# Kernel optimization log

Measured on AMD Instinct MI355X. Metric: run time of the kernel, lower is better.

The kernel has to match this reference:

```python
import jax, jax.numpy as jnp
import numpy as np

B, S, D, H = 4, 2048, 1024, 16
HD = D // H  # head_dim = 64


def setup_inputs() -> dict:
    key = jax.random.key(0)
    ks = jax.random.split(key, 9)
    sc = 1.0 / np.sqrt(D)
    return {
        "x": jax.random.normal(ks[0], (B, S, D), dtype=jnp.float32),
        "Wq": jax.random.normal(ks[1], (D, D), dtype=jnp.float32) * sc,
        "bq": jnp.zeros((D,), dtype=jnp.float32),
        "Wk": jax.random.normal(ks[2], (D, D), dtype=jnp.float32) * sc,
        "bk": jnp.zeros((D,), dtype=jnp.float32),
        "Wv": jax.random.normal(ks[3], (D, D), dtype=jnp.float32) * sc,
        "bv": jnp.zeros((D,), dtype=jnp.float32),
        "Wo": jax.random.normal(ks[4], (D, D), dtype=jnp.float32) * sc,
        "bo": jnp.zeros((D,), dtype=jnp.float32),
    }


def reference(x, Wq, bq, Wk, bk, Wv, bv, Wo, bo):
    # QKV projections (torch Linear: x @ W.T + b), reshape to [B, H, S, HD]
    def proj(W, b):
        return (x @ W.T + b).reshape(B, S, H, HD).transpose(0, 2, 1, 3)

    Q, K, V = proj(Wq, bq), proj(Wk, bk), proj(Wv, bv)
    scores = jnp.einsum("bhqd,bhkd->bhqk", Q, K) / jnp.sqrt(jnp.float32(HD))
    attn = jax.nn.softmax(scores, axis=-1)  # dropout is identity at eval
    ctx = jnp.einsum("bhqk,bhkd->bhqd", attn, V)
    ctx = ctx.transpose(0, 2, 1, 3).reshape(B, S, D)
    out = ctx @ Wo.T + bo
    return out, attn
```

## Files before the change

### kernel.cpp

```cpp
#include <hip/hip_runtime.h>
#include <stdint.h>

#define Mm 8192
#define Dd 1024

typedef unsigned short u16;
typedef __attribute__((ext_vector_type(8))) short bf16x8;
typedef __attribute__((ext_vector_type(4))) float f32x4;
typedef __attribute__((ext_vector_type(4))) u16 u16x4;

__device__ __forceinline__ u16 f2bf(float f) {
  union { float f; uint32_t u; } c; c.f = f;
  uint32_t u = c.u;
  return (u16)((u + 0x7fffu + ((u >> 16) & 1u)) >> 16);
}

__device__ __forceinline__ float EXP2(float x) {
#if __has_builtin(__builtin_amdgcn_exp2f)
  return __builtin_amdgcn_exp2f(x);
#else
  return exp2f(x);
#endif
}

__device__ __forceinline__ float LOG2(float x) {
#if __has_builtin(__builtin_amdgcn_logf)
  return __builtin_amdgcn_logf(x);
#else
  return log2f(x);
#endif
}

__device__ __forceinline__ uint32_t cvtpk(float a, float b) {
  uint32_t r;
  asm("v_cvt_pk_bf16_f32 %0, %1, %2" : "=v"(r) : "v"(a), "v"(b));
  return r;
}

__device__ __forceinline__ void gll16(const void* g, void* l) {
  __builtin_amdgcn_global_load_lds((const __attribute__((address_space(1))) void*)g,
                                   (__attribute__((address_space(3))) void*)l, 16, 0, 0);
}

__global__ void cvt_all(const float* __restrict__ x, const float* __restrict__ wq,
                        const float* __restrict__ wk, const float* __restrict__ wv,
                        const float* __restrict__ wo, u16* __restrict__ out) {
  const int xn4 = 2097152, wn4 = 262144;
  const int total = xn4 + 4 * wn4;
  int i = blockIdx.x * blockDim.x + threadIdx.x;
  int stride = gridDim.x * blockDim.x;
  for (; i < total; i += stride) {
    const float* src; int off;
    if (i < xn4) { src = x; off = i; }
    else {
      int j = i - xn4; int wsel = j >> 18; off = j & (wn4 - 1);
      src = (wsel == 0) ? wq : (wsel == 1) ? wk : (wsel == 2) ? wv : wo;
    }
    float4 v = ((const float4*)src)[off];
    u16x4 o;
    o.x = f2bf(v.x); o.y = f2bf(v.y); o.z = f2bf(v.z); o.w = f2bf(v.w);
    ((u16x4*)out)[i] = o;
  }
}

__global__ __launch_bounds__(256) void gemm_qkv(
    const u16* __restrict__ A, const u16* __restrict__ Wt,
    const float* __restrict__ bq, const float* __restrict__ bk, const float* __restrict__ bv,
    u16* __restrict__ Qo, u16* __restrict__ Ko, u16* __restrict__ Vo, float qscale)
{
  __shared__ u16 As[128 * 32];
  __shared__ u16 Bs[128 * 32];
  const int K = 1024, tiles_n = 24;
  int nwg = 64 * 24;
  int bid = blockIdx.x;
  { int q = nwg >> 3; bid = (bid & 7) * q + (bid >> 3); }
  int tm = bid / tiles_n, tn = bid % tiles_n;
  int tid = threadIdx.x;
  int wid = tid >> 6, lane = tid & 63;
  int wr = wid >> 1, wc = wid & 1;

  f32x4 acc[4][4] = {};
  int a_row = wr * 64 + (lane & 15);
  int b_row = wc * 64 + (lane & 15);
  int frag_k = (lane >> 4) * 8;

  const u16* ga0 = A + (size_t)(tm * 128 + wid * 32 + (lane >> 2)) * K + (lane & 3) * 8;
  const u16* ga1 = ga0 + (size_t)16 * K;
  const u16* gb0 = Wt + (size_t)(tn * 128 + wid * 32 + (lane >> 2)) * K + (lane & 3) * 8;
  const u16* gb1 = gb0 + (size_t)16 * K;
  u16* lA0 = As + wid * 1024;
  u16* lA1 = As + wid * 1024 + 512;
  u16* lB0 = Bs + wid * 1024;
  u16* lB1 = Bs + wid * 1024 + 512;

  for (int kt = 0; kt < K; kt += 32) {
    gll16(ga0 + kt, lA0);
    gll16(ga1 + kt, lA1);
    gll16(gb0 + kt, lB0);
    gll16(gb1 + kt, lB1);
    __syncthreads();
    bf16x8 af[4], bfr[4];
#pragma unroll
    for (int i = 0; i < 4; i++)
      af[i] = *(const bf16x8*)(As + (a_row + i * 16) * 32 + frag_k);
#pragma unroll
    for (int i = 0; i < 4; i++)
      bfr[i] = *(const bf16x8*)(Bs + (b_row + i * 16) * 32 + frag_k);
#pragma unroll
    for (int i = 0; i < 4; i++)
#pragma unroll
      for (int j = 0; j < 4; j++)
        acc[i][j] = __builtin_amdgcn_mfma_f32_16x16x32_bf16(af[i], bfr[j], acc[i][j], 0, 0, 0);
    __syncthreads();
  }

#pragma unroll
  for (int i = 0; i < 4; i++) {
#pragma unroll
    for (int j = 0; j < 4; j++) {
      int col = tn * 128 + wc * 64 + j * 16 + (lane & 15);
      int wsel = col >> 10, c10 = col & 1023;
      int h = c10 >> 6, hd = c10 & 63;
      float bvv = (wsel == 0 ? bq : wsel == 1 ? bk : bv)[c10];
      int row0 = tm * 128 + wr * 64 + i * 16 + (lane >> 4) * 4;
      int b_ = row0 >> 11, s0 = row0 & 2047;
      if (wsel == 2) {
        u16x4 o;
#pragma unroll
        for (int r = 0; r < 4; r++) o[r] = f2bf(acc[i][j][r] + bvv);
        *(u16x4*)&Vo[((size_t)(b_ * 16 + h) * 64 + hd) * 2048 + s0] = o;
      } else {
        u16* dst = (wsel == 0) ? Qo : Ko;
        float sc = (wsel == 0) ? qscale : 1.0f;
#pragma unroll
        for (int r = 0; r < 4; r++)
          dst[(((size_t)(b_ * 16 + h) * 2048 + (s0 + r)) << 6) + hd] = f2bf((acc[i][j][r] + bvv) * sc);
      }
    }
  }
}

__global__ __launch_bounds__(256) void gemm_out(
    const u16* __restrict__ A, const u16* __restrict__ Bt,
    const float* __restrict__ bias, float* __restrict__ out,
    int M, int N, int K)
{
  __shared__ u16 As[128 * 32];
  __shared__ u16 Bs[128 * 32];
  int tiles_n = N >> 7;
  int nwg = (M >> 7) * tiles_n;
  int bid = blockIdx.x;
  { int q = nwg >> 3; bid = (bid & 7) * q + (bid >> 3); }
  int tm = bid / tiles_n, tn = bid % tiles_n;
  int tid = threadIdx.x;
  int wid = tid >> 6, lane = tid & 63;
  int wr = wid >> 1, wc = wid & 1;

  f32x4 acc[4][4] = {};
  int a_row = wr * 64 + (lane & 15);
  int b_row = wc * 64 + (lane & 15);
  int frag_k = (lane >> 4) * 8;

  const u16* ga0 = A + (size_t)(tm * 128 + wid * 32 + (lane >> 2)) * K + (lane & 3) * 8;
  const u16* ga1 = ga0 + (size_t)16 * K;
  const u16* gb0 = Bt + (size_t)(tn * 128 + wid * 32 + (lane >> 2)) * K + (lane & 3) * 8;
  const u16* gb1 = gb0 + (size_t)16 * K;
  u16* lA0 = As + wid * 1024;
  u16* lA1 = As + wid * 1024 + 512;
  u16* lB0 = Bs + wid * 1024;
  u16* lB1 = Bs + wid * 1024 + 512;

  for (int kt = 0; kt < K; kt += 32) {
    gll16(ga0 + kt, lA0);
    gll16(ga1 + kt, lA1);
    gll16(gb0 + kt, lB0);
    gll16(gb1 + kt, lB1);
    __syncthreads();
    bf16x8 af[4], bfr[4];
#pragma unroll
    for (int i = 0; i < 4; i++)
      af[i] = *(const bf16x8*)(As + (a_row + i * 16) * 32 + frag_k);
#pragma unroll
    for (int i = 0; i < 4; i++)
      bfr[i] = *(const bf16x8*)(Bs + (b_row + i * 16) * 32 + frag_k);
#pragma unroll
    for (int i = 0; i < 4; i++)
#pragma unroll
      for (int j = 0; j < 4; j++)
        acc[i][j] = __builtin_amdgcn_mfma_f32_16x16x32_bf16(af[i], bfr[j], acc[i][j], 0, 0, 0);
    __syncthreads();
  }

#pragma unroll
  for (int i = 0; i < 4; i++)
#pragma unroll
    for (int j = 0; j < 4; j++) {
      int col = tn * 128 + wc * 64 + j * 16 + (lane & 15);
      float bv = bias[col];
#pragma unroll
      for (int r = 0; r < 4; r++) {
        int row = tm * 128 + wr * 64 + i * 16 + (lane >> 4) * 4 + r;
        out[(size_t)row * N + col] = acc[i][j][r] + bv;
      }
    }
}

__global__ __launch_bounds__(512, 4) void attn_fused16q2(
    const u16* __restrict__ Qb, const u16* __restrict__ Kb,
    const u16* __restrict__ Vtb, float* __restrict__ attn_out,
    u16* __restrict__ ctxb)
{
  __shared__ u16 Ks[4][4096];
  __shared__ u16 Vs[4][4096];
  __shared__ u16 Ps[8192];

  int bid = blockIdx.x;
  int swz = (bid & 7) * 64 + (bid >> 3);
  int bh = swz >> 3, qtb = swz & 7;
  int tid = threadIdx.x, w = tid >> 6, lane = tid & 63;
  int g = lane >> 4, l15 = lane & 15;

  const u16* Kg = Kb + (size_t)bh * 2048 * 64;
  const u16* Vg = Vtb + (size_t)bh * 64 * 2048;
  const u16* Qg = Qb + ((size_t)bh * 2048 + qtb * 256) * 64;
  float* Ag = attn_out + ((size_t)bh * 2048 + qtb * 256) * 2048;

  int qloc = w * 16 + l15;
  bf16x8 aqA0 = *(const bf16x8*)(Qg + (size_t)qloc * 64 + g * 8);
  bf16x8 aqA1 = *(const bf16x8*)(Qg + (size_t)qloc * 64 + 32 + g * 8);
  bf16x8 aqB0 = *(const bf16x8*)(Qg + (size_t)(128 + qloc) * 64 + g * 8);
  bf16x8 aqB1 = *(const bf16x8*)(Qg + (size_t)(128 + qloc) * 64 + 32 + g * 8);

  int srow = w * 8 + (lane >> 3);
  int schunk = (lane & 7) ^ (lane >> 3);
  const u16* Ksrc = Kg + (size_t)srow * 64 + schunk * 8;
  const u16* Vsrc = Vg + (size_t)srow * 2048 + schunk * 8;

  int xq = (qloc & 7) << 4;
  char* Pb = (char*)Ps + qloc * 128;

  float eA0 = 0.f, eA1 = 0.f, eB0 = 0.f, eB1 = 0.f;
#pragma unroll
  for (int p = 0; p < 3; p++)
    gll16(Ksrc + (size_t)p * 4096, (char*)Ks[p] + w * 1024);
  for (int it = 0; it < 32; ++it) {
    if (it < 29) gll16(Ksrc + (size_t)(it + 3) * 4096, (char*)Ks[(it + 3) & 3] + w * 1024);
    if (it < 29)       asm volatile("s_waitcnt vmcnt(3)" ::: "memory");
    else if (it == 29) asm volatile("s_waitcnt vmcnt(2)" ::: "memory");
    else if (it == 30) asm volatile("s_waitcnt vmcnt(1)" ::: "memory");
    else               asm volatile("s_waitcnt vmcnt(0)" ::: "memory");
    __builtin_amdgcn_s_barrier();
    const char* Kbase = (const char*)Ks[it & 3];
    f32x4 sA[4] = {}, sB[4] = {};
    __builtin_amdgcn_s_setprio(1);
#pragma unroll
    for (int t = 0; t < 4; t++) {
      int kr = t * 16 + l15;
      int x = (kr & 7) << 4;
      bf16x8 k0 = *(const bf16x8*)(Kbase + kr * 128 + ((g * 16) ^ x));
      bf16x8 k1 = *(const bf16x8*)(Kbase + kr * 128 + ((64 + g * 16) ^ x));
      sA[t] = __builtin_amdgcn_mfma_f32_16x16x32_bf16(k0, aqA0, sA[t], 0, 0, 0);
      sA[t] = __builtin_amdgcn_mfma_f32_16x16x32_bf16(k1, aqA1, sA[t], 0, 0, 0);
      sB[t] = __builtin_amdgcn_mfma_f32_16x16x32_bf16(k0, aqB0, sB[t], 0, 0, 0);
      sB[t] = __builtin_amdgcn_mfma_f32_16x16x32_bf16(k1, aqB1, sB[t], 0, 0, 0);
    }
    __builtin_amdgcn_s_setprio(0);
#pragma unroll
    for (int t = 0; t < 4; t++)
#pragma unroll
      for (int r = 0; r < 4; r++) {
        if (t & 1) { eA1 += EXP2(sA[t][r]); eB1 += EXP2(sB[t][r]); }
        else       { eA0 += EXP2(sA[t][r]); eB0 += EXP2(sB[t][r]); }
      }
    asm volatile("" ::: "memory");
    __builtin_amdgcn_s_barrier();
  }
  float lsA = eA0 + eA1, lsB = eB0 + eB1;
  lsA += __shfl_xor(lsA, 16); lsA += __shfl_xor(lsA, 32);
  lsB += __shfl_xor(lsB, 16); lsB += __shfl_xor(lsB, 32);
  float lrA = -LOG2(lsA), lrB = -LOG2(lsB);

  f32x4 cA[4] = {}, cB[4] = {};
#pragma unroll
  for (int p = 0; p < 3; p++) {
    gll16(Ksrc + (size_t)p * 4096, (char*)Ks[p] + w * 1024);
    gll16(Vsrc + (size_t)p * 64,  (char*)Vs[p] + w * 1024);
  }
  for (int it = 0; it < 32; ++it) {
    if (it < 29) {
      gll16(Ksrc + (size_t)(it + 3) * 4096, (char*)Ks[(it + 3) & 3] + w * 1024);
      gll16(Vsrc + (size_t)(it + 3) * 64,  (char*)Vs[(it + 3) & 3] + w * 1024);
    }
    if (it == 0)      asm volatile("s_waitcnt vmcnt(6)" ::: "memory");
    else if (it == 1) asm volatile("s_waitcnt vmcnt(14)" ::: "memory");
    else if (it == 2) asm volatile("s_waitcnt vmcnt(22)" ::: "memory");
    else if (it < 29) asm volatile("s_waitcnt vmcnt(30)" ::: "memory");
    else if (it == 29) asm volatile("s_waitcnt vmcnt(28)" ::: "memory");
    else if (it == 30) asm volatile("s_waitcnt vmcnt(26)" ::: "memory");
    else               asm volatile("s_waitcnt vmcnt(24)" ::: "memory");
    __builtin_amdgcn_s_barrier();
    const char* Kbase = (const char*)Ks[it & 3];
    const char* Vbase = (const char*)Vs[it & 3];
    f32x4 sA[4] = {}, sB[4] = {};
    __builtin_amdgcn_s_setprio(1);
#pragma unroll
    for (int t = 0; t < 4; t++) {
      int kr = t * 16 + l15;
      int x = (kr & 7) << 4;
      bf16x8 k0 = *(const bf16x8*)(Kbase + kr * 128 + ((g * 16) ^ x));
      bf16x8 k1 = *(const bf16x8*)(Kbase + kr * 128 + ((64 + g * 16) ^ x));
      sA[t] = __builtin_amdgcn_mfma_f32_16x16x32_bf16(k0, aqA0, sA[t], 0, 0, 0);
      sA[t] = __builtin_amdgcn_mfma_f32_16x16x32_bf16(k1, aqA1, sA[t], 0, 0, 0);
      sB[t] = __builtin_amdgcn_mfma_f32_16x16x32_bf16(k0, aqB0, sB[t], 0, 0, 0);
      sB[t] = __builtin_amdgcn_mfma_f32_16x16x32_bf16(k1, aqB1, sB[t], 0, 0, 0);
    }
    __builtin_amdgcn_s_setprio(0);

    {
      float* Arow = Ag + (size_t)qloc * 2048 + it * 64 + g * 4;
#pragma unroll
      for (int t = 0; t < 4; t++) {
        f32x4 p;
#pragma unroll
        for (int r = 0; r < 4; r++) p[r] = EXP2(sA[t][r] + lrA);
        __builtin_nontemporal_store(p, (f32x4*)(Arow + t * 16));
        uint2 pk;
        pk.x = cvtpk(p[0], p[1]);
        pk.y = cvtpk(p[2], p[3]);
        *(uint2*)(Pb + ((t * 32 + g * 8) ^ xq)) = pk;
      }
      __builtin_amdgcn_s_setprio(1);
#pragma unroll
      for (int kk = 0; kk < 2; kk++) {
        bf16x8 ap = *(const bf16x8*)(Pb + ((kk * 64 + g * 16) ^ xq));
#pragma unroll
        for (int t = 0; t < 4; t++) {
          int dr = t * 16 + l15;
          bf16x8 bv = *(const bf16x8*)(Vbase + dr * 128 + ((kk * 64 + g * 16) ^ ((dr & 7) << 4)));
          cA[t] = __builtin_amdgcn_mfma_f32_16x16x32_bf16(ap, bv, cA[t], 0, 0, 0);
        }
      }
      __builtin_amdgcn_s_setprio(0);
    }
    {
      float* Arow = Ag + (size_t)(128 + qloc) * 2048 + it * 64 + g * 4;
#pragma unroll
      for (int t = 0; t < 4; t++) {
        f32x4 p;
#pragma unroll
        for (int r = 0; r < 4; r++) p[r] = EXP2(sB[t][r] + lrB);
        __builtin_nontemporal_store(p, (f32x4*)(Arow + t * 16));
        uint2 pk;
        pk.x = cvtpk(p[0], p[1]);
        pk.y = cvtpk(p[2], p[3]);
        *(uint2*)(Pb + ((t * 32 + g * 8) ^ xq)) = pk;
      }
      __builtin_amdgcn_s_setprio(1);
#pragma unroll
      for (int kk = 0; kk < 2; kk++) {
        bf16x8 ap = *(const bf16x8*)(Pb + ((kk * 64 + g * 16) ^ xq));
#pragma unroll
        for (int t = 0; t < 4; t++) {
          int dr = t * 16 + l15;
          bf16x8 bv = *(const bf16x8*)(Vbase + dr * 128 + ((kk * 64 + g * 16) ^ ((dr & 7) << 4)));
          cB[t] = __builtin_amdgcn_mfma_f32_16x16x32_bf16(ap, bv, cB[t], 0, 0, 0);
        }
      }
      __builtin_amdgcn_s_setprio(0);
    }
    asm volatile("" ::: "memory");
    __builtin_amdgcn_s_barrier();
  }

  int b_ = bh >> 4, h = bh & 15;
#pragma unroll
  for (int t = 0; t < 4; t++)
#pragma unroll
    for (int r = 0; r < 4; r++) {
      int qgA = qtb * 256 + w * 16 + g * 4 + r;
      int col = h * 64 + t * 16 + l15;
      ctxb[((size_t)b_ * 2048 + qgA) * 1024 + col] = f2bf(cA[t][r]);
      ctxb[((size_t)b_ * 2048 + qgA + 128) * 1024 + col] = f2bf(cB[t][r]);
    }
}

extern "C" void kernel_launch(void* const* d_in, const int* in_sizes, int n_in,
                              void* d_out, int out_size, void* d_ws, size_t ws_size,
                              hipStream_t stream) {
  const float* x  = (const float*)d_in[0];
  const float* Wq = (const float*)d_in[1];
  const float* bq = (const float*)d_in[2];
  const float* Wk = (const float*)d_in[3];
  const float* bk = (const float*)d_in[4];
  const float* Wv = (const float*)d_in[5];
  const float* bv = (const float*)d_in[6];
  const float* Wo = (const float*)d_in[7];
  const float* bo = (const float*)d_in[8];

  u16* xb   = (u16*)d_ws;
  u16* Wqb  = xb + (size_t)Mm * Dd;
  u16* Wkb  = Wqb + (size_t)Dd * Dd;
  u16* Wvb  = Wkb + (size_t)Dd * Dd;
  u16* Wob  = Wvb + (size_t)Dd * Dd;
  u16* Qb   = Wob + (size_t)Dd * Dd;
  u16* Kbuf = Qb + (size_t)Mm * Dd;
  u16* Vtb  = Kbuf + (size_t)Mm * Dd;
  u16* ctxb = Vtb + (size_t)Mm * Dd;

  float* out_f = (float*)d_out;
  float* attn_o = out_f + (size_t)Mm * Dd;

  cvt_all<<<2048, 256, 0, stream>>>(x, Wq, Wk, Wv, Wo, xb);

  const float qscale = 0.125f * 1.44269504088896340736f;
  gemm_qkv<<<1536, 256, 0, stream>>>(xb, Wqb, bq, bk, bv, Qb, Kbuf, Vtb, qscale);
  attn_fused16q2<<<512, 512, 0, stream>>>(Qb, Kbuf, Vtb, attn_o, ctxb);
  gemm_out<<<512, 256, 0, stream>>>(ctxb, Wob, bo, out_f, Mm, Dd, Dd);
}
```

Baseline: 495.0 us.

## Split fused attention into separate row-sum and probability/context kernels

The single fused attention kernel, which handled 256 queries per block in two sequential phases, is replaced by two kernels of 1024 blocks with 128 queries each. The first computes the per-row log-sum-exp normaliser and writes it to a workspace buffer. The second reloads it, then writes probabilities and accumulates the context. The aim is more blocks, fewer registers per block and a higher occupancy target for the reduction pass, with shallower prefetch and fewer barriers. In exchange, K tiles are loaded from global memory twice as often per query, and there is an extra launch and a small global round-trip for the normaliser.

```diff
diff --git a/kernel.cpp b/kernel.cpp
--- a/kernel.cpp
+++ b/kernel.cpp
@@ -205,53 +205,37 @@
     }
 }
 
-__global__ __launch_bounds__(512, 4) void attn_fused16q2(
-    const u16* __restrict__ Qb, const u16* __restrict__ Kb,
-    const u16* __restrict__ Vtb, float* __restrict__ attn_out,
-    u16* __restrict__ ctxb)
+__global__ __launch_bounds__(512, 8) void attn_pass1(
+    const u16* __restrict__ Qb, const u16* __restrict__ Kb, float* __restrict__ lrbuf)
 {
   __shared__ u16 Ks[4][4096];
-  __shared__ u16 Vs[4][4096];
-  __shared__ u16 Ps[8192];
-
   int bid = blockIdx.x;
-  int swz = (bid & 7) * 64 + (bid >> 3);
-  int bh = swz >> 3, qtb = swz & 7;
+  int swz = (bid & 7) * 128 + (bid >> 3);
+  int bh = swz >> 4, qt = swz & 15;
   int tid = threadIdx.x, w = tid >> 6, lane = tid & 63;
   int g = lane >> 4, l15 = lane & 15;
 
+  const u16* Qg = Qb + ((size_t)bh * 2048 + qt * 128) * 64;
   const u16* Kg = Kb + (size_t)bh * 2048 * 64;
-  const u16* Vg = Vtb + (size_t)bh * 64 * 2048;
-  const u16* Qg = Qb + ((size_t)bh * 2048 + qtb * 256) * 64;
-  float* Ag = attn_out + ((size_t)bh * 2048 + qtb * 256) * 2048;
-
   int qloc = w * 16 + l15;
-  bf16x8 aqA0 = *(const bf16x8*)(Qg + (size_t)qloc * 64 + g * 8);
-  bf16x8 aqA1 = *(const bf16x8*)(Qg + (size_t)qloc * 64 + 32 + g * 8);
-  bf16x8 aqB0 = *(const bf16x8*)(Qg + (size_t)(128 + qloc) * 64 + g * 8);
-  bf16x8 aqB1 = *(const bf16x8*)(Qg + (size_t)(128 + qloc) * 64 + 32 + g * 8);
+  bf16x8 aq0 = *(const bf16x8*)(Qg + (size_t)qloc * 64 + g * 8);
+  bf16x8 aq1 = *(const bf16x8*)(Qg + (size_t)qloc * 64 + 32 + g * 8);
 
   int srow = w * 8 + (lane >> 3);
   int schunk = (lane & 7) ^ (lane >> 3);
   const u16* Ksrc = Kg + (size_t)srow * 64 + schunk * 8;
-  const u16* Vsrc = Vg + (size_t)srow * 2048 + schunk * 8;
-
-  int xq = (qloc & 7) << 4;
-  char* Pb = (char*)Ps + qloc * 128;
-
-  float eA0 = 0.f, eA1 = 0.f, eB0 = 0.f, eB1 = 0.f;
-#pragma unroll
-  for (int p = 0; p < 3; p++)
-    gll16(Ksrc + (size_t)p * 4096, (char*)Ks[p] + w * 1024);
+
+  float ls0 = 0.f, ls1 = 0.f, ls2 = 0.f, ls3 = 0.f;
+  gll16(Ksrc, (char*)Ks[0] + w * 1024);
+  gll16(Ksrc + 4096, (char*)Ks[1] + w * 1024);
   for (int it = 0; it < 32; ++it) {
-    if (it < 29) gll16(Ksrc + (size_t)(it + 3) * 4096, (char*)Ks[(it + 3) & 3] + w * 1024);
-    if (it < 29)       asm volatile("s_waitcnt vmcnt(3)" ::: "memory");
-    else if (it == 29) asm volatile("s_waitcnt vmcnt(2)" ::: "memory");
+    if (it < 30) gll16(Ksrc + (size_t)(it + 2) * 4096, (char*)Ks[(it + 2) & 3] + w * 1024);
+    if (it < 30)       asm volatile("s_waitcnt vmcnt(2)" ::: "memory");
     else if (it == 30) asm volatile("s_waitcnt vmcnt(1)" ::: "memory");
     else               asm volatile("s_waitcnt vmcnt(0)" ::: "memory");
     __builtin_amdgcn_s_barrier();
     const char* Kbase = (const char*)Ks[it & 3];
-    f32x4 sA[4] = {}, sB[4] = {};
+    f32x4 s[4] = {};
     __builtin_amdgcn_s_setprio(1);
 #pragma unroll
     for (int t = 0; t < 4; t++) {
@@ -259,49 +243,75 @@
       int x = (kr & 7) << 4;
       bf16x8 k0 = *(const bf16x8*)(Kbase + kr * 128 + ((g * 16) ^ x));
       bf16x8 k1 = *(const bf16x8*)(Kbase + kr * 128 + ((64 + g * 16) ^ x));
-      sA[t] = __builtin_amdgcn_mfma_f32_16x16x32_bf16(k0, aqA0, sA[t], 0, 0, 0);
-      sA[t] = __builtin_amdgcn_mfma_f32_16x16x32_bf16(k1, aqA1, sA[t], 0, 0, 0);
-      sB[t] = __builtin_amdgcn_mfma_f32_16x16x32_bf16(k0, aqB0, sB[t], 0, 0, 0);
-      sB[t] = __builtin_amdgcn_mfma_f32_16x16x32_bf16(k1, aqB1, sB[t], 0, 0, 0);
+      s[t] = __builtin_amdgcn_mfma_f32_16x16x32_bf16(k0, aq0, s[t], 0, 0, 0);
+      s[t] = __builtin_amdgcn_mfma_f32_16x16x32_bf16(k1, aq1, s[t], 0, 0, 0);
     }
     __builtin_amdgcn_s_setprio(0);
 #pragma unroll
-    for (int t = 0; t < 4; t++)
-#pragma unroll
-      for (int r = 0; r < 4; r++) {
-        if (t & 1) { eA1 += EXP2(sA[t][r]); eB1 += EXP2(sB[t][r]); }
-        else       { eA0 += EXP2(sA[t][r]); eB0 += EXP2(sB[t][r]); }
-      }
-    asm volatile("" ::: "memory");
-    __builtin_amdgcn_s_barrier();
-  }
-  float lsA = eA0 + eA1, lsB = eB0 + eB1;
-  lsA += __shfl_xor(lsA, 16); lsA += __shfl_xor(lsA, 32);
-  lsB += __shfl_xor(lsB, 16); lsB += __shfl_xor(lsB, 32);
-  float lrA = -LOG2(lsA), lrB = -LOG2(lsB);
-
-  f32x4 cA[4] = {}, cB[4] = {};
-#pragma unroll
-  for (int p = 0; p < 3; p++) {
+    for (int r = 0; r < 4; r++) {
+      ls0 += EXP2(s[0][r]); ls1 += EXP2(s[1][r]);
+      ls2 += EXP2(s[2][r]); ls3 += EXP2(s[3][r]);
+    }
+  }
+  float lsum = (ls0 + ls1) + (ls2 + ls3);
+  lsum += __shfl_xor(lsum, 16);
+  lsum += __shfl_xor(lsum, 32);
+  if (!g) lrbuf[(size_t)bh * 2048 + qt * 128 + qloc] = -LOG2(lsum);
+}
+
+__global__ __launch_bounds__(512, 4) void attn_pass2(
+    const u16* __restrict__ Qb, const u16* __restrict__ Kb,
+    const u16* __restrict__ Vtb, const float* __restrict__ lrbuf,
+    float* __restrict__ attn_out, u16* __restrict__ ctxb)
+{
+  __shared__ u16 Ks[4][4096];
+  __shared__ u16 Vs[4][4096];
+  __shared__ u16 Ps[8192];
+
+  int bid = blockIdx.x;
+  int swz = (bid & 7) * 128 + (bid >> 3);
+  int bh = swz >> 4, qt = swz & 15;
+  int tid = threadIdx.x, w = tid >> 6, lane = tid & 63;
+  int g = lane >> 4, l15 = lane & 15;
+
+  const u16* Qg = Qb + ((size_t)bh * 2048 + qt * 128) * 64;
+  const u16* Kg = Kb + (size_t)bh * 2048 * 64;
+  const u16* Vg = Vtb + (size_t)bh * 64 * 2048;
+  float* Ag = attn_out + ((size_t)bh * 2048 + qt * 128) * 2048;
+
+  int qloc = w * 16 + l15;
+  bf16x8 aq0 = *(const bf16x8*)(Qg + (size_t)qloc * 64 + g * 8);
+  bf16x8 aq1 = *(const bf16x8*)(Qg + (size_t)qloc * 64 + 32 + g * 8);
+  float lr2 = lrbuf[(size_t)bh * 2048 + qt * 128 + qloc];
+
+  int srow = w * 8 + (lane >> 3);
+  int schunk = (lane & 7) ^ (lane >> 3);
+  const u16* Ksrc = Kg + (size_t)srow * 64 + schunk * 8;
+  const u16* Vsrc = Vg + (size_t)srow * 2048 + schunk * 8;
+
+  int xq = (qloc & 7) << 4;
+  char* Pb = (char*)Ps + qloc * 128;
+
+  f32x4 ctx[4] = {};
+#pragma unroll
+  for (int p = 0; p < 2; p++) {
     gll16(Ksrc + (size_t)p * 4096, (char*)Ks[p] + w * 1024);
     gll16(Vsrc + (size_t)p * 64,  (char*)Vs[p] + w * 1024);
   }
   for (int it = 0; it < 32; ++it) {
-    if (it < 29) {
-      gll16(Ksrc + (size_t)(it + 3) * 4096, (char*)Ks[(it + 3) & 3] + w * 1024);
-      gll16(Vsrc + (size_t)(it + 3) * 64,  (char*)Vs[(it + 3) & 3] + w * 1024);
-    }
-    if (it == 0)      asm volatile("s_waitcnt vmcnt(6)" ::: "memory");
-    else if (it == 1) asm volatile("s_waitcnt vmcnt(14)" ::: "memory");
-    else if (it == 2) asm volatile("s_waitcnt vmcnt(22)" ::: "memory");
-    else if (it < 29) asm volatile("s_waitcnt vmcnt(30)" ::: "memory");
-    else if (it == 29) asm volatile("s_waitcnt vmcnt(28)" ::: "memory");
-    else if (it == 30) asm volatile("s_waitcnt vmcnt(26)" ::: "memory");
-    else               asm volatile("s_waitcnt vmcnt(24)" ::: "memory");
+    if (it < 30) {
+      gll16(Ksrc + (size_t)(it + 2) * 4096, (char*)Ks[(it + 2) & 3] + w * 1024);
+      gll16(Vsrc + (size_t)(it + 2) * 64,  (char*)Vs[(it + 2) & 3] + w * 1024);
+    }
+    if (it == 0)       asm volatile("s_waitcnt vmcnt(4)" ::: "memory");
+    else if (it == 1)  asm volatile("s_waitcnt vmcnt(8)" ::: "memory");
+    else if (it < 30)  asm volatile("s_waitcnt vmcnt(12)" ::: "memory");
+    else if (it == 30) asm volatile("s_waitcnt vmcnt(10)" ::: "memory");
+    else               asm volatile("s_waitcnt vmcnt(8)" ::: "memory");
     __builtin_amdgcn_s_barrier();
     const char* Kbase = (const char*)Ks[it & 3];
     const char* Vbase = (const char*)Vs[it & 3];
-    f32x4 sA[4] = {}, sB[4] = {};
+    f32x4 s[4] = {};
     __builtin_amdgcn_s_setprio(1);
 #pragma unroll
     for (int t = 0; t < 4; t++) {
@@ -309,67 +319,34 @@
       int x = (kr & 7) << 4;
       bf16x8 k0 = *(const bf16x8*)(Kbase + kr * 128 + ((g * 16) ^ x));
       bf16x8 k1 = *(const bf16x8*)(Kbase + kr * 128 + ((64 + g * 16) ^ x));
-      sA[t] = __builtin_amdgcn_mfma_f32_16x16x32_bf16(k0, aqA0, sA[t], 0, 0, 0);
-      sA[t] = __builtin_amdgcn_mfma_f32_16x16x32_bf16(k1, aqA1, sA[t], 0, 0, 0);
-      sB[t] = __builtin_amdgcn_mfma_f32_16x16x32_bf16(k0, aqB0, sB[t], 0, 0, 0);
-      sB[t] = __builtin_amdgcn_mfma_f32_16x16x32_bf16(k1, aqB1, sB[t], 0, 0, 0);
+      s[t] = __builtin_amdgcn_mfma_f32_16x16x32_bf16(k0, aq0, s[t], 0, 0, 0);
+      s[t] = __builtin_amdgcn_mfma_f32_16x16x32_bf16(k1, aq1, s[t], 0, 0, 0);
     }
     __builtin_amdgcn_s_setprio(0);
-
-    {
-      float* Arow = Ag + (size_t)qloc * 2048 + it * 64 + g * 4;
+    float* Arow = Ag + (size_t)qloc * 2048 + it * 64 + g * 4;
+#pragma unroll
+    for (int t = 0; t < 4; t++) {
+      f32x4 p;
+#pragma unroll
+      for (int r = 0; r < 4; r++) p[r] = EXP2(s[t][r] + lr2);
+      __builtin_nontemporal_store(p, (f32x4*)(Arow + t * 16));
+      uint2 pk;
+      pk.x = cvtpk(p[0], p[1]);
+      pk.y = cvtpk(p[2], p[3]);
+      *(uint2*)(Pb + ((t * 32 + g * 8) ^ xq)) = pk;
+    }
+    __builtin_amdgcn_s_setprio(1);
+#pragma unroll
+    for (int kk = 0; kk < 2; kk++) {
+      bf16x8 ap = *(const bf16x8*)(Pb + ((kk * 64 + g * 16) ^ xq));
 #pragma unroll
       for (int t = 0; t < 4; t++) {
-        f32x4 p;
-#pragma unroll
-        for (int r = 0; r < 4; r++) p[r] = EXP2(sA[t][r] + lrA);
-        __builtin_nontemporal_store(p, (f32x4*)(Arow + t * 16));
-        uint2 pk;
-        pk.x = cvtpk(p[0], p[1]);
-        pk.y = cvtpk(p[2], p[3]);
-        *(uint2*)(Pb + ((t * 32 + g * 8) ^ xq)) = pk;
+        int dr = t * 16 + l15;
+        bf16x8 bv = *(const bf16x8*)(Vbase + dr * 128 + ((kk * 64 + g * 16) ^ ((dr & 7) << 4)));
+        ctx[t] = __builtin_amdgcn_mfma_f32_16x16x32_bf16(ap, bv, ctx[t], 0, 0, 0);
       }
-      __builtin_amdgcn_s_setprio(1);
-#pragma unroll
-      for (int kk = 0; kk < 2; kk++) {
-        bf16x8 ap = *(const bf16x8*)(Pb + ((kk * 64 + g * 16) ^ xq));
-#pragma unroll
-        for (int t = 0; t < 4; t++) {
-          int dr = t * 16 + l15;
-          bf16x8 bv = *(const bf16x8*)(Vbase + dr * 128 + ((kk * 64 + g * 16) ^ ((dr & 7) << 4)));
-          cA[t] = __builtin_amdgcn_mfma_f32_16x16x32_bf16(ap, bv, cA[t], 0, 0, 0);
-        }
-      }
-      __builtin_amdgcn_s_setprio(0);
-    }
-    {
-      float* Arow = Ag + (size_t)(128 + qloc) * 2048 + it * 64 + g * 4;
-#pragma unroll
-      for (int t = 0; t < 4; t++) {
-        f32x4 p;
-#pragma unroll
-        for (int r = 0; r < 4; r++) p[r] = EXP2(sB[t][r] + lrB);
-        __builtin_nontemporal_store(p, (f32x4*)(Arow + t * 16));
-        uint2 pk;
-        pk.x = cvtpk(p[0], p[1]);
-        pk.y = cvtpk(p[2], p[3]);
-        *(uint2*)(Pb + ((t * 32 + g * 8) ^ xq)) = pk;
-      }
-      __builtin_amdgcn_s_setprio(1);
-#pragma unroll
-      for (int kk = 0; kk < 2; kk++) {
-        bf16x8 ap = *(const bf16x8*)(Pb + ((kk * 64 + g * 16) ^ xq));
-#pragma unroll
-        for (int t = 0; t < 4; t++) {
-          int dr = t * 16 + l15;
-          bf16x8 bv = *(const bf16x8*)(Vbase + dr * 128 + ((kk * 64 + g * 16) ^ ((dr & 7) << 4)));
-          cB[t] = __builtin_amdgcn_mfma_f32_16x16x32_bf16(ap, bv, cB[t], 0, 0, 0);
-        }
-      }
-      __builtin_amdgcn_s_setprio(0);
-    }
-    asm volatile("" ::: "memory");
-    __builtin_amdgcn_s_barrier();
+    }
+    __builtin_amdgcn_s_setprio(0);
   }
 
   int b_ = bh >> 4, h = bh & 15;
@@ -377,10 +354,9 @@
   for (int t = 0; t < 4; t++)
 #pragma unroll
     for (int r = 0; r < 4; r++) {
-      int qgA = qtb * 256 + w * 16 + g * 4 + r;
+      int qg = qt * 128 + w * 16 + g * 4 + r;
       int col = h * 64 + t * 16 + l15;
-      ctxb[((size_t)b_ * 2048 + qgA) * 1024 + col] = f2bf(cA[t][r]);
-      ctxb[((size_t)b_ * 2048 + qgA + 128) * 1024 + col] = f2bf(cB[t][r]);
+      ctxb[((size_t)b_ * 2048 + qg) * 1024 + col] = f2bf(ctx[t][r]);
     }
 }
 
@@ -406,6 +382,7 @@
   u16* Kbuf = Qb + (size_t)Mm * Dd;
   u16* Vtb  = Kbuf + (size_t)Mm * Dd;
   u16* ctxb = Vtb + (size_t)Mm * Dd;
+  float* lrbuf = (float*)(ctxb + (size_t)Mm * Dd);
 
   float* out_f = (float*)d_out;
   float* attn_o = out_f + (size_t)Mm * Dd;
@@ -414,6 +391,7 @@
 
   const float qscale = 0.125f * 1.44269504088896340736f;
   gemm_qkv<<<1536, 256, 0, stream>>>(xb, Wqb, bq, bk, bv, Qb, Kbuf, Vtb, qscale);
-  attn_fused16q2<<<512, 512, 0, stream>>>(Qb, Kbuf, Vtb, attn_o, ctxb);
+  attn_pass1<<<1024, 512, 0, stream>>>(Qb, Kbuf, lrbuf);
+  attn_pass2<<<1024, 512, 0, stream>>>(Qb, Kbuf, Vtb, lrbuf, attn_o, ctxb);
   gemm_out<<<512, 256, 0, stream>>>(ctxb, Wob, bo, out_f, Mm, Dd, Dd);
 }
```

Result: slower. 509.0 us (+2.8%).
